# Optimization experiments

Measured on AMD Instinct MI355X. Metric: run time of the kernel, lower is better.

## Reference

```python
import jax, jax.numpy as jnp
import numpy as np

N = 50000      # number of nodes
D = 128        # embedding dim
K = 16         # padded neighbors per node
B = 100000     # number of train pairs
LAYERS = 2     # convolution layers


def setup_inputs() -> dict:
    key = jax.random.key(0)
    k_pairs, k_lab, k_nbr, k_emb, k_w1, k_w2 = jax.random.split(key, 6)
    pairs = jax.random.randint(k_pairs, (B, 2), 0, N, dtype=jnp.int64 if jax.config.jax_enable_x64 else jnp.int32)
    labels = jax.random.randint(k_lab, (B,), 0, 2, dtype=jnp.int32)
    neighbors = jax.random.randint(k_nbr, (N, K), 0, N, dtype=jnp.int32)
    embedding = jax.random.normal(k_emb, (N, D), dtype=jnp.float32)
    W1 = jax.random.normal(k_w1, (2 * D, D), dtype=jnp.float32) * (1.0 / np.sqrt(2 * D))
    b1 = jnp.zeros((D,), dtype=jnp.float32)
    W2 = jax.random.normal(k_w2, (D, 2), dtype=jnp.float32) * (1.0 / np.sqrt(D))
    b2 = jnp.zeros((2,), dtype=jnp.float32)
    return {"pairs": pairs, "labels": labels, "neighbors": neighbors,
            "embedding": embedding, "W1": W1, "b1": b1, "W2": W2, "b2": b2}


def _aggregate(embedding, neighbors):
    # Multi-layer mean neighbor aggregation over all N nodes.
    H = embedding
    for _ in range(LAYERS):
        # gather [N, K, D] then mean over neighbors -> [N, D]
        H = jnp.take(H, neighbors, axis=0).mean(axis=1)
    return H


def reference(pairs, labels, neighbors, embedding, W1, b1, W2, b2):
    H = _aggregate(embedding, neighbors)           # [N, D]
    src = jnp.take(H, pairs[:, 0], axis=0)         # [B, D]
    dst = jnp.take(H, pairs[:, 1], axis=0)         # [B, D]
    x = jnp.concatenate([src, dst], axis=-1)       # [B, 2D]
    h = jax.nn.relu(x @ W1 + b1)                   # [B, D]
    logits = h @ W2 + b2                           # [B, 2]
    # Original applies Softmax, then CrossEntropyLoss (which log_softmaxes again).
    probs = jax.nn.softmax(logits, axis=-1)
    logp = jax.nn.log_softmax(probs, axis=-1)
    loss = -jnp.take_along_axis(logp, labels[:, None].astype(jnp.int32), axis=1).mean()
    return loss
```

## Files before the change

### kernel.cpp

```cpp
#include <hip/hip_runtime.h>
#include <hip/hip_bf16.h>

#define NNODES 50000
#define DIM    128
#define KNBR   16
#define NPAIRS 100000
#define MBLK   64
#define NT     1563
#define GRID_P 512

typedef float          f32x4  __attribute__((ext_vector_type(4)));
typedef float          f32x2  __attribute__((ext_vector_type(2)));
typedef __bf16         bf16x8 __attribute__((ext_vector_type(8)));
typedef unsigned short u16x8  __attribute__((ext_vector_type(8)));
typedef unsigned int   u32x2  __attribute__((ext_vector_type(2)));
typedef unsigned int   u32x4  __attribute__((ext_vector_type(4)));

__device__ __forceinline__ unsigned short f2bf(float f) {
    unsigned int u = __builtin_bit_cast(unsigned int, f);
    u = (u + 0x7fffu + ((u >> 16) & 1u)) >> 16;
    return (unsigned short)u;
}

#if __has_builtin(__builtin_amdgcn_cvt_pk_f32_fp8) && __has_builtin(__builtin_amdgcn_cvt_pk_fp8_f32)
template <bool HI>
__device__ __forceinline__ f32x2 fp8x2_dec(unsigned int w) {
    return __builtin_amdgcn_cvt_pk_f32_fp8((int)w, HI);
}
template <bool HI>
__device__ __forceinline__ unsigned int fp8x2_enc(float a, float b, unsigned int old) {
    return (unsigned int)__builtin_amdgcn_cvt_pk_fp8_f32(a, b, (int)old, HI);
}
#else
__device__ __forceinline__ float e4m3_dec1(unsigned int b) {
    unsigned int s = (b & 0x80u) << 24;
    unsigned int em = b & 0x7fu;
    float mag = (em >= 8u)
        ? __builtin_bit_cast(float, (((em >> 3) + 120u) << 23) | ((em & 7u) << 20))
        : (float)em * 0.001953125f;
    return __builtin_bit_cast(float, __builtin_bit_cast(unsigned int, mag) | s);
}
template <bool HI>
__device__ __forceinline__ f32x2 fp8x2_dec(unsigned int w) {
    unsigned int v = HI ? (w >> 16) : w;
    f32x2 r; r[0] = e4m3_dec1(v & 0xffu); r[1] = e4m3_dec1((v >> 8) & 0xffu);
    return r;
}
__device__ __forceinline__ unsigned int e4m3_enc1(float f) {
    unsigned int s = (__builtin_bit_cast(unsigned int, f) >> 24) & 0x80u;
    float af = fminf(fabsf(f), 448.0f);
    unsigned int u = __builtin_bit_cast(unsigned int, af);
    int e = (int)(u >> 23) - 127;
    if (e < -9) return s;
    if (e < -6) { int q = (int)rintf(af * 512.0f); return s | (unsigned int)q; }
    unsigned int mant = u & 0x7fffffu;
    unsigned int r = (mant + 0x7ffffu + ((mant >> 20) & 1u)) >> 20;
    unsigned int out = (((unsigned int)(e + 7)) << 3) + r;
    if (out > 0x7eu) out = 0x7eu;
    return s | out;
}
template <bool HI>
__device__ __forceinline__ unsigned int fp8x2_enc(float a, float b, unsigned int old) {
    unsigned int p = e4m3_enc1(a) | (e4m3_enc1(b) << 8);
    return HI ? ((old & 0x0000ffffu) | (p << 16)) : ((old & 0xffff0000u) | p);
}
#endif

#define AS1 __attribute__((address_space(1)))
#define AS3 __attribute__((address_space(3)))
__device__ __forceinline__ void gload_lds16(const void* g, void* l) {
    __builtin_amdgcn_global_load_lds((AS1 void*)(g), (AS3 void*)(l), 16, 0, 0);
}

__global__ void w1t_kernel(const float* __restrict__ W1, unsigned short* __restrict__ W1t) {
    int g = blockIdx.x * 256 + threadIdx.x;
    int i = g >> 7;
    int d = g & 127;
    W1t[d * 256 + i] = f2bf(W1[g]);
}

__global__ void e2f8_kernel(const float* __restrict__ E, unsigned int* __restrict__ E8) {
    int g = blockIdx.x * 256 + threadIdx.x;
    const f32x4 v0 = *(const f32x4*)(E + (size_t)g * 8);
    const f32x4 v1 = *(const f32x4*)(E + (size_t)g * 8 + 4);
    unsigned int w0 = 0, w1 = 0;
    w0 = fp8x2_enc<false>(v0[0], v0[1], w0);
    w0 = fp8x2_enc<true >(v0[2], v0[3], w0);
    w1 = fp8x2_enc<false>(v1[0], v1[1], w1);
    w1 = fp8x2_enc<true >(v1[2], v1[3], w1);
    u32x2 o; o[0] = w0; o[1] = w1;
    *(u32x2*)(E8 + (size_t)g * 2) = o;
}

__device__ __forceinline__ void agg_core(const unsigned char* __restrict__ T,
                                         const int* __restrict__ nbr,
                                         unsigned char* lds_wave,
                                         int node_base,
                                         int lane, float* a ) {
    const int rsub = lane >> 3;
    const int bcol = (lane & 7) * 16;
    const int* nb = nbr + node_base * KNBR;
#pragma unroll
    for (int i = 0; i < 8; ++i) {
        int nl = nb[i * 8 + rsub];
        gload_lds16(T + (size_t)nl * 128 + bcol, lds_wave + i * 1024);
    }
    asm volatile("s_waitcnt vmcnt(0)" ::: "memory");
    __builtin_amdgcn_sched_barrier(0);
    const int g = lane >> 4;
    const int c = lane & 15;
#pragma unroll
    for (int j = 0; j < 8; ++j) a[j] = 0.f;
#pragma unroll
    for (int k = 0; k < KNBR; ++k) {
        const u32x2 v = *(const u32x2*)(lds_wave + (g * 16 + k) * 128 + c * 8);
        f32x2 f;
        f = fp8x2_dec<false>(v[0]); a[0] += f[0]; a[1] += f[1];
        f = fp8x2_dec<true >(v[0]); a[2] += f[0]; a[3] += f[1];
        f = fp8x2_dec<false>(v[1]); a[4] += f[0]; a[5] += f[1];
        f = fp8x2_dec<true >(v[1]); a[6] += f[0]; a[7] += f[1];
    }
}

__global__ __launch_bounds__(256) void agg1_kernel(const unsigned char* __restrict__ E8,
                                                   const int* __restrict__ nbr,
                                                   unsigned char* __restrict__ H1f8) {
    __shared__ unsigned char SL[4][8192];
    const int t = threadIdx.x, wave = t >> 6, lane = t & 63;
    const int node_base = blockIdx.x * 16 + wave * 4;
    float a[8];
    agg_core(E8, nbr, SL[wave], node_base, lane, a);
    const int g = lane >> 4, c = lane & 15;
    unsigned int o0 = 0, o1 = 0;
    o0 = fp8x2_enc<false>(a[0] * 0.0625f, a[1] * 0.0625f, o0);
    o0 = fp8x2_enc<true >(a[2] * 0.0625f, a[3] * 0.0625f, o0);
    o1 = fp8x2_enc<false>(a[4] * 0.0625f, a[5] * 0.0625f, o1);
    o1 = fp8x2_enc<true >(a[6] * 0.0625f, a[7] * 0.0625f, o1);
    u32x2 o; o[0] = o0; o[1] = o1;
    *(u32x2*)(H1f8 + (size_t)(node_base + g) * 128 + c * 8) = o;
}

__global__ __launch_bounds__(256) void agg2_kernel(const unsigned char* __restrict__ H1f8,
                                                   const int* __restrict__ nbr,
                                                   unsigned short* __restrict__ H2b) {
    __shared__ unsigned char SL[4][8192];
    const int t = threadIdx.x, wave = t >> 6, lane = t & 63;
    const int node_base = blockIdx.x * 16 + wave * 4;
    float a[8];
    agg_core(H1f8, nbr, SL[wave], node_base, lane, a);
    const int g = lane >> 4, c = lane & 15;
    u16x8 o;
#pragma unroll
    for (int j = 0; j < 8; ++j) o[j] = f2bf(a[j] * 0.0625f);
    *(u16x8*)(H2b + (size_t)(node_base + g) * DIM + c * 8) = o;
}

__global__ __launch_bounds__(256, 2) void pair_mlp_kernel(
    const int* __restrict__ pairs, const int* __restrict__ labels,
    const unsigned short* __restrict__ H2b, const unsigned short* __restrict__ W1t,
    const float* __restrict__ b1, const float* __restrict__ W2,
    const float* __restrict__ b2, float* __restrict__ out) {
    __shared__ unsigned short As[2][MBLK * 256];
    __shared__ float LP[4][MBLK][2];
    __shared__ float wred[4];

    const int tid  = threadIdx.x;
    const int wave = tid >> 6;
    const int lane = tid & 63;
    const int bid  = blockIdx.x;

    const int lq   = (lane & 31) * 16;
    const int lr   = lane >> 5;
    const int half = lq >> 8;
    const int lg   = lane >> 4;
    const int ll   = lane & 15;
    const int col0 = wave * 32 + ll;
    const int col1 = col0 + 16;
    const int myN  = (NT - bid + GRID_P - 1) / GRID_P;

    const float b1v0 = b1[col0], b1v1 = b1[col1];
    const float w2a0 = W2[col0 * 2], w2b0 = W2[col0 * 2 + 1];
    const float w2a1 = W2[col1 * 2], w2b1 = W2[col1 * 2 + 1];
    const float b20 = b2[0], b21 = b2[1];
    int lab[4] = {0, 0, 0, 0};
#pragma unroll
    for (int j = 0; j < 4; ++j) {
        int tt = bid + j * GRID_P;
        if (tt < NT && tid < MBLK) {
            int pm = tt * MBLK + tid;
            if (pm < NPAIRS) lab[j] = labels[pm];
        }
    }
    bf16x8 breg0[8], breg1[8];
#pragma unroll
    for (int ks = 0; ks < 8; ++ks) {
        const int kb = ks * 64 + lg * 16;
        breg0[ks] = *(const bf16x8*)((const char*)W1t + col0 * 512 + kb);
        breg1[ks] = *(const bf16x8*)((const char*)W1t + col1 * 512 + kb);
    }
#pragma unroll
    for (int i = 0; i < 8; ++i) {
        int m0 = wave * 16 + i * 2;
        int m  = m0 + lr;
        int b  = lq ^ ((m & 7) << 4);
        int pm = bid * MBLK + m; if (pm >= NPAIRS) pm = NPAIRS - 1;
        int node = pairs[pm * 2 + half];
        gload_lds16((const char*)H2b + (size_t)node * 256 + (b & 255),
                    (char*)&As[0][0] + m0 * 512);
    }

    float lacc = 0.f;
#pragma unroll
    for (int j = 0; j < 4; ++j) {
        const int t = bid + j * GRID_P;
        if (t >= NT) break;
        int tn = t + GRID_P; if (tn >= NT) tn = t;
        const int cur = j & 1;

        asm volatile("s_waitcnt vmcnt(0)" ::: "memory");
        __builtin_amdgcn_sched_barrier(0);
        __builtin_amdgcn_s_barrier();
        __builtin_amdgcn_sched_barrier(0);

        int nd[8];
#pragma unroll
        for (int i = 0; i < 8; ++i) {
            int m  = wave * 16 + i * 2 + lr;
            int pm = tn * MBLK + m; if (pm >= NPAIRS) pm = NPAIRS - 1;
            nd[i] = pairs[pm * 2 + half];
        }

        f32x4 acc[4][2];
        {
            f32x4 z = {0.f, 0.f, 0.f, 0.f};
#pragma unroll
            for (int i = 0; i < 4; ++i) { acc[i][0] = z; acc[i][1] = z; }
        }
#pragma unroll
        for (int ks = 0; ks < 8; ++ks) {
            const int kb = ks * 64 + lg * 16;
#pragma unroll
            for (int mf = 0; mf < 4; ++mf) {
                int row = mf * 16 + ll;
                bf16x8 af = *(const bf16x8*)((const char*)&As[cur][0] + row * 512 + (kb ^ ((row & 7) << 4)));
                acc[mf][0] = __builtin_amdgcn_mfma_f32_16x16x32_bf16(af, breg0[ks], acc[mf][0], 0, 0, 0);
                acc[mf][1] = __builtin_amdgcn_mfma_f32_16x16x32_bf16(af, breg1[ks], acc[mf][1], 0, 0, 0);
            }
        }

#pragma unroll
        for (int i = 0; i < 8; ++i) {
            int m0 = wave * 16 + i * 2;
            int m  = m0 + lr;
            int b  = lq ^ ((m & 7) << 4);
            gload_lds16((const char*)H2b + (size_t)nd[i] * 256 + (b & 255),
                        (char*)&As[cur ^ 1][0] + m0 * 512);
        }

#pragma unroll
        for (int mf = 0; mf < 4; ++mf) {
            float p0[4], p1[4];
#pragma unroll
            for (int r = 0; r < 4; ++r) {
                float h0 = fmaxf(acc[mf][0][r] + b1v0, 0.f);
                float h1 = fmaxf(acc[mf][1][r] + b1v1, 0.f);
                p0[r] = h0 * w2a0 + h1 * w2a1;
                p1[r] = h0 * w2b0 + h1 * w2b1;
            }
#pragma unroll
            for (int s = 1; s < 16; s <<= 1) {
#pragma unroll
                for (int r = 0; r < 4; ++r) {
                    p0[r] += __shfl_xor(p0[r], s, 16);
                    p1[r] += __shfl_xor(p1[r], s, 16);
                }
            }
            if (ll == 0) {
                int rb = mf * 16 + lg * 4;
#pragma unroll
                for (int r = 0; r < 4; ++r) {
                    LP[wave][rb + r][0] = p0[r];
                    LP[wave][rb + r][1] = p1[r];
                }
            }
        }
        asm volatile("s_waitcnt lgkmcnt(0)" ::: "memory");
        __builtin_amdgcn_sched_barrier(0);
        __builtin_amdgcn_s_barrier();
        __builtin_amdgcn_sched_barrier(0);

        if (tid < MBLK) {
            int pm = t * MBLK + tid;
            if (pm < NPAIRS) {
                float l0 = b20 + LP[0][tid][0] + LP[1][tid][0] + LP[2][tid][0] + LP[3][tid][0];
                float l1 = b21 + LP[0][tid][1] + LP[1][tid][1] + LP[2][tid][1] + LP[3][tid][1];
                float mx = fmaxf(l0, l1);
                float e0 = __expf(l0 - mx), e1 = __expf(l1 - mx);
                float inv = 1.f / (e0 + e1);
                float q0 = e0 * inv, q1 = e1 * inv;
                float lse2 = __logf(__expf(q0) + __expf(q1));
                lacc += lse2 - (lab[j] ? q1 : q0);
            }
        }
    }

    __syncthreads();
#pragma unroll
    for (int s = 1; s < 64; s <<= 1) lacc += __shfl_xor(lacc, s, 64);
    if (lane == 0) wred[wave] = lacc;
    __syncthreads();
    if (tid == 0)
        atomicAdd(out, (wred[0] + wred[1] + wred[2] + wred[3]) * (1.0f / (float)NPAIRS));
}

extern "C" void kernel_launch(void* const* d_in, const int* in_sizes, int n_in,
                              void* d_out, int out_size, void* d_ws, size_t ws_size,
                              hipStream_t stream) {
    const int*   pairs  = (const int*)d_in[0];
    const int*   labels = (const int*)d_in[1];
    const int*   nbr    = (const int*)d_in[2];
    const float* E      = (const float*)d_in[3];
    const float* W1     = (const float*)d_in[4];
    const float* b1     = (const float*)d_in[5];
    const float* W2     = (const float*)d_in[6];
    const float* b2     = (const float*)d_in[7];
    float* out = (float*)d_out;

    char* ws = (char*)d_ws;
    unsigned short* W1t  = (unsigned short*)(ws);
    unsigned char*  E8   = (unsigned char*)(ws + 65536);
    unsigned char*  H1f8 = E8 + (size_t)NNODES * DIM;
    unsigned short* H2b  = (unsigned short*)(H1f8 + (size_t)NNODES * DIM);

    (void)hipMemsetAsync(out, 0, sizeof(float), stream);

    w1t_kernel<<<dim3(128), dim3(256), 0, stream>>>(W1, W1t);
    e2f8_kernel<<<dim3((NNODES * DIM) / (256 * 8)), dim3(256), 0, stream>>>(E, (unsigned int*)E8);
    agg1_kernel<<<dim3(NNODES / 16), dim3(256), 0, stream>>>(E8, nbr, H1f8);
    agg2_kernel<<<dim3(NNODES / 16), dim3(256), 0, stream>>>(H1f8, nbr, H2b);
    pair_mlp_kernel<<<dim3(GRID_P), dim3(256), 0, stream>>>(
        pairs, labels, H2b, W1t, b1, W2, b2, out);
}
```

Measured before the change: 140.3 us.

## Precompute per-node W1 projections then gather them per pair for the loss

Splits x@W1 into H@W1_top and H@W1_bottom, computed once per node (50k rows) in a new MFMA GEMM kernel and stored as bf16 P|Q. The per-pair kernel then gathers P[src] and Q[dst], adds them, and applies ReLU, the W2 dot product and the loss. This halves the GEMM FLOPs (50k×256 outputs instead of 100k×128×2) and replaces the per-pair GEMM with a cheap gather, at the cost of an extra 25.6MB intermediate write and read and bf16 rounding of P and Q. It also folds the output memset into the W1 transpose kernel.

```diff
diff --git a/kernel.cpp b/kernel.cpp
--- a/kernel.cpp
+++ b/kernel.cpp
@@ -5,16 +5,14 @@
 #define DIM    128
 #define KNBR   16
 #define NPAIRS 100000
-#define MBLK   64
-#define NT     1563
-#define GRID_P 512
+#define PBLK   1250
+#define PITER  5
 
 typedef float          f32x4  __attribute__((ext_vector_type(4)));
 typedef float          f32x2  __attribute__((ext_vector_type(2)));
 typedef __bf16         bf16x8 __attribute__((ext_vector_type(8)));
 typedef unsigned short u16x8  __attribute__((ext_vector_type(8)));
 typedef unsigned int   u32x2  __attribute__((ext_vector_type(2)));
-typedef unsigned int   u32x4  __attribute__((ext_vector_type(4)));
 
 __device__ __forceinline__ unsigned short f2bf(float f) {
     unsigned int u = __builtin_bit_cast(unsigned int, f);
@@ -72,11 +70,13 @@
     __builtin_amdgcn_global_load_lds((AS1 void*)(g), (AS3 void*)(l), 16, 0, 0);
 }
 
-__global__ void w1t_kernel(const float* __restrict__ W1, unsigned short* __restrict__ W1t) {
+__global__ void w1t_kernel(const float* __restrict__ W1, unsigned short* __restrict__ W1t,
+                           float* __restrict__ out) {
     int g = blockIdx.x * 256 + threadIdx.x;
     int i = g >> 7;
     int d = g & 127;
     W1t[d * 256 + i] = f2bf(W1[g]);
+    if (g == 0) out[0] = 0.f;
 }
 
 __global__ void e2f8_kernel(const float* __restrict__ E, unsigned int* __restrict__ E8) {
@@ -95,8 +95,7 @@
 __device__ __forceinline__ void agg_core(const unsigned char* __restrict__ T,
                                          const int* __restrict__ nbr,
                                          unsigned char* lds_wave,
-                                         int node_base,
-                                         int lane, float* a ) {
+                                         int node_base, int lane, float* a) {
     const int rsub = lane >> 3;
     const int bcol = (lane & 7) * 16;
     const int* nb = nbr + node_base * KNBR;
@@ -155,162 +154,134 @@
     *(u16x8*)(H2b + (size_t)(node_base + g) * DIM + c * 8) = o;
 }
 
-__global__ __launch_bounds__(256, 2) void pair_mlp_kernel(
+__global__ __launch_bounds__(256, 2) void gemmpq_kernel(
+    const unsigned short* __restrict__ H2b, const unsigned short* __restrict__ W1t,
+    unsigned short* __restrict__ PQb) {
+    __shared__ unsigned char  Ast[64 * 256];
+    __shared__ unsigned short Cbuf[64 * 256];
+
+    const int tid = threadIdx.x, wave = tid >> 6, lane = tid & 63;
+    const int lg = lane >> 4, ll = lane & 15;
+    const int rowbase = blockIdx.x * 64;
+
+    {
+        const int lq = (lane & 15) * 16;
+        const int lr = lane >> 4;
+#pragma unroll
+        for (int i = 0; i < 4; ++i) {
+            int r0 = wave * 16 + i * 4;
+            int row = r0 + lr;
+            int grow = rowbase + row; if (grow >= NNODES) grow = NNODES - 1;
+            int b = lq ^ ((row & 7) << 4);
+            gload_lds16((const char*)H2b + (size_t)grow * 256 + b, Ast + r0 * 256);
+        }
+    }
+
+    const int qoff = (wave >= 2) ? 256 : 0;
+    bf16x8 breg[4][4];
+#pragma unroll
+    for (int cg = 0; cg < 4; ++cg) {
+        int jj = (wave * 64 + cg * 16 + ll) & 127;
+#pragma unroll
+        for (int ks = 0; ks < 4; ++ks)
+            breg[cg][ks] = *(const bf16x8*)((const char*)W1t + jj * 512 + qoff + ks * 64 + lg * 16);
+    }
+    __syncthreads();
+
+    f32x4 acc[4][4];
+    {
+        f32x4 z = {0.f, 0.f, 0.f, 0.f};
+#pragma unroll
+        for (int i = 0; i < 4; ++i)
+#pragma unroll
+            for (int j = 0; j < 4; ++j) acc[i][j] = z;
+    }
+#pragma unroll
+    for (int ks = 0; ks < 4; ++ks) {
+#pragma unroll
+        for (int mf = 0; mf < 4; ++mf) {
+            int row = mf * 16 + ll;
+            bf16x8 af = *(const bf16x8*)(Ast + row * 256 + ((ks * 64 + lg * 16) ^ ((row & 7) << 4)));
+#pragma unroll
+            for (int cg = 0; cg < 4; ++cg)
+                acc[mf][cg] = __builtin_amdgcn_mfma_f32_16x16x32_bf16(af, breg[cg][ks], acc[mf][cg], 0, 0, 0);
+        }
+    }
+
+#pragma unroll
+    for (int mf = 0; mf < 4; ++mf)
+#pragma unroll
+        for (int cg = 0; cg < 4; ++cg) {
+            int col = wave * 64 + cg * 16 + ll;
+#pragma unroll
+            for (int r = 0; r < 4; ++r)
+                Cbuf[(mf * 16 + lg * 4 + r) * 256 + col] = f2bf(acc[mf][cg][r]);
+        }
+    __syncthreads();
+#pragma unroll
+    for (int it = 0; it < 8; ++it) {
+        int c = tid + it * 256;
+        int row = c >> 5, cw = c & 31;
+        int grow = rowbase + row;
+        if (grow < NNODES)
+            *(u16x8*)((char*)PQb + (size_t)grow * 512 + cw * 16) =
+                *(const u16x8*)((const char*)Cbuf + row * 512 + cw * 16);
+    }
+}
+
+__global__ __launch_bounds__(256) void pair_loss_kernel(
     const int* __restrict__ pairs, const int* __restrict__ labels,
-    const unsigned short* __restrict__ H2b, const unsigned short* __restrict__ W1t,
-    const float* __restrict__ b1, const float* __restrict__ W2,
-    const float* __restrict__ b2, float* __restrict__ out) {
-    __shared__ unsigned short As[2][MBLK * 256];
-    __shared__ float LP[4][MBLK][2];
-    __shared__ float wred[4];
-
-    const int tid  = threadIdx.x;
-    const int wave = tid >> 6;
-    const int lane = tid & 63;
-    const int bid  = blockIdx.x;
-
-    const int lq   = (lane & 31) * 16;
-    const int lr   = lane >> 5;
-    const int half = lq >> 8;
-    const int lg   = lane >> 4;
-    const int ll   = lane & 15;
-    const int col0 = wave * 32 + ll;
-    const int col1 = col0 + 16;
-    const int myN  = (NT - bid + GRID_P - 1) / GRID_P;
-
-    const float b1v0 = b1[col0], b1v1 = b1[col1];
-    const float w2a0 = W2[col0 * 2], w2b0 = W2[col0 * 2 + 1];
-    const float w2a1 = W2[col1 * 2], w2b1 = W2[col1 * 2 + 1];
+    const unsigned short* __restrict__ PQb, const float* __restrict__ b1,
+    const float* __restrict__ W2, const float* __restrict__ b2,
+    float* __restrict__ out) {
+    __shared__ float sred[4];
+    const int tid = threadIdx.x, wave = tid >> 6, lane = tid & 63;
+    const int pg = lane >> 4, c = lane & 15;
+
+    float b1c[8], w2a[8], w2b[8];
+#pragma unroll
+    for (int j = 0; j < 8; ++j) {
+        b1c[j] = b1[c * 8 + j];
+        w2a[j] = W2[(c * 8 + j) * 2];
+        w2b[j] = W2[(c * 8 + j) * 2 + 1];
+    }
     const float b20 = b2[0], b21 = b2[1];
-    int lab[4] = {0, 0, 0, 0};
-#pragma unroll
-    for (int j = 0; j < 4; ++j) {
-        int tt = bid + j * GRID_P;
-        if (tt < NT && tid < MBLK) {
-            int pm = tt * MBLK + tid;
-            if (pm < NPAIRS) lab[j] = labels[pm];
-        }
-    }
-    bf16x8 breg0[8], breg1[8];
-#pragma unroll
-    for (int ks = 0; ks < 8; ++ks) {
-        const int kb = ks * 64 + lg * 16;
-        breg0[ks] = *(const bf16x8*)((const char*)W1t + col0 * 512 + kb);
-        breg1[ks] = *(const bf16x8*)((const char*)W1t + col1 * 512 + kb);
-    }
-#pragma unroll
-    for (int i = 0; i < 8; ++i) {
-        int m0 = wave * 16 + i * 2;
-        int m  = m0 + lr;
-        int b  = lq ^ ((m & 7) << 4);
-        int pm = bid * MBLK + m; if (pm >= NPAIRS) pm = NPAIRS - 1;
-        int node = pairs[pm * 2 + half];
-        gload_lds16((const char*)H2b + (size_t)node * 256 + (b & 255),
-                    (char*)&As[0][0] + m0 * 512);
-    }
 
     float lacc = 0.f;
 #pragma unroll
-    for (int j = 0; j < 4; ++j) {
-        const int t = bid + j * GRID_P;
-        if (t >= NT) break;
-        int tn = t + GRID_P; if (tn >= NT) tn = t;
-        const int cur = j & 1;
-
-        asm volatile("s_waitcnt vmcnt(0)" ::: "memory");
-        __builtin_amdgcn_sched_barrier(0);
-        __builtin_amdgcn_s_barrier();
-        __builtin_amdgcn_sched_barrier(0);
-
-        int nd[8];
-#pragma unroll
-        for (int i = 0; i < 8; ++i) {
-            int m  = wave * 16 + i * 2 + lr;
-            int pm = tn * MBLK + m; if (pm >= NPAIRS) pm = NPAIRS - 1;
-            nd[i] = pairs[pm * 2 + half];
-        }
-
-        f32x4 acc[4][2];
-        {
-            f32x4 z = {0.f, 0.f, 0.f, 0.f};
-#pragma unroll
-            for (int i = 0; i < 4; ++i) { acc[i][0] = z; acc[i][1] = z; }
-        }
-#pragma unroll
-        for (int ks = 0; ks < 8; ++ks) {
-            const int kb = ks * 64 + lg * 16;
-#pragma unroll
-            for (int mf = 0; mf < 4; ++mf) {
-                int row = mf * 16 + ll;
-                bf16x8 af = *(const bf16x8*)((const char*)&As[cur][0] + row * 512 + (kb ^ ((row & 7) << 4)));
-                acc[mf][0] = __builtin_amdgcn_mfma_f32_16x16x32_bf16(af, breg0[ks], acc[mf][0], 0, 0, 0);
-                acc[mf][1] = __builtin_amdgcn_mfma_f32_16x16x32_bf16(af, breg1[ks], acc[mf][1], 0, 0, 0);
-            }
-        }
-
-#pragma unroll
-        for (int i = 0; i < 8; ++i) {
-            int m0 = wave * 16 + i * 2;
-            int m  = m0 + lr;
-            int b  = lq ^ ((m & 7) << 4);
-            gload_lds16((const char*)H2b + (size_t)nd[i] * 256 + (b & 255),
-                        (char*)&As[cur ^ 1][0] + m0 * 512);
-        }
-
-#pragma unroll
-        for (int mf = 0; mf < 4; ++mf) {
-            float p0[4], p1[4];
-#pragma unroll
-            for (int r = 0; r < 4; ++r) {
-                float h0 = fmaxf(acc[mf][0][r] + b1v0, 0.f);
-                float h1 = fmaxf(acc[mf][1][r] + b1v1, 0.f);
-                p0[r] = h0 * w2a0 + h1 * w2a1;
-                p1[r] = h0 * w2b0 + h1 * w2b1;
-            }
-#pragma unroll
-            for (int s = 1; s < 16; s <<= 1) {
-#pragma unroll
-                for (int r = 0; r < 4; ++r) {
-                    p0[r] += __shfl_xor(p0[r], s, 16);
-                    p1[r] += __shfl_xor(p1[r], s, 16);
-                }
-            }
-            if (ll == 0) {
-                int rb = mf * 16 + lg * 4;
-#pragma unroll
-                for (int r = 0; r < 4; ++r) {
-                    LP[wave][rb + r][0] = p0[r];
-                    LP[wave][rb + r][1] = p1[r];
-                }
-            }
-        }
-        asm volatile("s_waitcnt lgkmcnt(0)" ::: "memory");
-        __builtin_amdgcn_sched_barrier(0);
-        __builtin_amdgcn_s_barrier();
-        __builtin_amdgcn_sched_barrier(0);
-
-        if (tid < MBLK) {
-            int pm = t * MBLK + tid;
-            if (pm < NPAIRS) {
-                float l0 = b20 + LP[0][tid][0] + LP[1][tid][0] + LP[2][tid][0] + LP[3][tid][0];
-                float l1 = b21 + LP[0][tid][1] + LP[1][tid][1] + LP[2][tid][1] + LP[3][tid][1];
-                float mx = fmaxf(l0, l1);
-                float e0 = __expf(l0 - mx), e1 = __expf(l1 - mx);
-                float inv = 1.f / (e0 + e1);
-                float q0 = e0 * inv, q1 = e1 * inv;
-                float lse2 = __logf(__expf(q0) + __expf(q1));
-                lacc += lse2 - (lab[j] ? q1 : q0);
-            }
-        }
-    }
-
-    __syncthreads();
-#pragma unroll
-    for (int s = 1; s < 64; s <<= 1) lacc += __shfl_xor(lacc, s, 64);
-    if (lane == 0) wred[wave] = lacc;
+    for (int it = 0; it < PITER; ++it) {
+        int p = (blockIdx.x + it * PBLK) * 16 + wave * 4 + pg;
+        int s = pairs[p * 2], d = pairs[p * 2 + 1];
+        bf16x8 pb = *(const bf16x8*)((const char*)PQb + (size_t)s * 512 + c * 16);
+        bf16x8 qb = *(const bf16x8*)((const char*)PQb + (size_t)d * 512 + 256 + c * 16);
+        float l0 = 0.f, l1 = 0.f;
+#pragma unroll
+        for (int j = 0; j < 8; ++j) {
+            float h = fmaxf((float)pb[j] + (float)qb[j] + b1c[j], 0.f);
+            l0 += h * w2a[j];
+            l1 += h * w2b[j];
+        }
+#pragma unroll
+        for (int sdist = 1; sdist < 16; sdist <<= 1) {
+            l0 += __shfl_xor(l0, sdist, 16);
+            l1 += __shfl_xor(l1, sdist, 16);
+        }
+        if (c == 0) {
+            l0 += b20; l1 += b21;
+            float mx = fmaxf(l0, l1);
+            float e0 = __expf(l0 - mx), e1 = __expf(l1 - mx);
+            float inv = 1.f / (e0 + e1);
+            float q0 = e0 * inv, q1 = e1 * inv;
+            float lse2 = __logf(__expf(q0) + __expf(q1));
+            lacc += lse2 - (labels[p] ? q1 : q0);
+        }
+    }
+#pragma unroll
+    for (int sdist = 1; sdist < 64; sdist <<= 1) lacc += __shfl_xor(lacc, sdist, 64);
+    if (lane == 0) sred[wave] = lacc;
     __syncthreads();
     if (tid == 0)
-        atomicAdd(out, (wred[0] + wred[1] + wred[2] + wred[3]) * (1.0f / (float)NPAIRS));
+        atomicAdd(out, (sred[0] + sred[1] + sred[2] + sred[3]) * (1.0f / (float)NPAIRS));
 }
 
 extern "C" void kernel_launch(void* const* d_in, const int* in_sizes, int n_in,
@@ -328,16 +299,15 @@
 
     char* ws = (char*)d_ws;
     unsigned short* W1t  = (unsigned short*)(ws);
-    unsigned char*  E8   = (unsigned char*)(ws + 65536);
-    unsigned char*  H1f8 = E8 + (size_t)NNODES * DIM;
-    unsigned short* H2b  = (unsigned short*)(H1f8 + (size_t)NNODES * DIM);
-
-    (void)hipMemsetAsync(out, 0, sizeof(float), stream);
-
-    w1t_kernel<<<dim3(128), dim3(256), 0, stream>>>(W1, W1t);
+    unsigned short* H2b  = (unsigned short*)(ws + 65536);
+    unsigned char*  E8   = (unsigned char*)(ws + 65536 + 12800000);
+    unsigned char*  H1f8 = E8 + 6400000;
+    unsigned short* PQb  = (unsigned short*)E8;
+
+    w1t_kernel<<<dim3(128), dim3(256), 0, stream>>>(W1, W1t, out);
     e2f8_kernel<<<dim3((NNODES * DIM) / (256 * 8)), dim3(256), 0, stream>>>(E, (unsigned int*)E8);
     agg1_kernel<<<dim3(NNODES / 16), dim3(256), 0, stream>>>(E8, nbr, H1f8);
     agg2_kernel<<<dim3(NNODES / 16), dim3(256), 0, stream>>>(H1f8, nbr, H2b);
-    pair_mlp_kernel<<<dim3(GRID_P), dim3(256), 0, stream>>>(
-        pairs, labels, H2b, W1t, b1, W2, b2, out);
-}
+    gemmpq_kernel<<<dim3((NNODES + 63) / 64), dim3(256), 0, stream>>>(H2b, W1t, PQb);
+    pair_loss_kernel<<<dim3(PBLK), dim3(256), 0, stream>>>(pairs, labels, PQb, b1, W2, b2, out);
+}
```

After: 152.2 us. +8.5%, slower.
